# Kernel tuning notes

Hardware: AMD Instinct MI355X
Metric: run time of the kernel (lower is better)

The kernel has to match this reference:

```python
import jax, jax.numpy as jnp
import numpy as np

HEADS = 16
DIM_HEAD = 64
SCALE = float(np.sqrt(DIM_HEAD))  # NOTE: original code MULTIPLIES by sqrt(dim_head)


def setup_inputs() -> dict:
    key = jax.random.key(0)
    k1, k2, k3, k4 = jax.random.split(key, 4)
    dim = 1024
    b, n = 2, 2048
    s = 1.0 / np.sqrt(dim)
    return {
        "x": jax.random.normal(k1, (b, n, dim), dtype=jnp.float32),
        "w_q": jax.random.normal(k2, (dim, HEADS * DIM_HEAD), dtype=jnp.float32) * s,
        "w_vk": jax.random.normal(k3, (dim, HEADS * DIM_HEAD * 2), dtype=jnp.float32) * s,
        "w_out": jax.random.normal(k4, (HEADS * DIM_HEAD, dim), dtype=jnp.float32) * s,
    }


def reference(x, w_q, w_vk, w_out):
    b, n, _ = x.shape
    h, d = HEADS, DIM_HEAD
    context = x  # context=None, kv_include_self=False
    q = (x @ w_q).reshape(b, n, h, d).transpose(0, 2, 1, 3)          # b h n d
    kv = context @ w_vk                                              # b n 2hd
    k, v = jnp.split(kv, 2, axis=-1)                                 # chunk order: k first, v second
    k = k.reshape(b, n, h, d).transpose(0, 2, 1, 3)
    v = v.reshape(b, n, h, d).transpose(0, 2, 1, 3)
    dots = jnp.einsum('bhid,bhjd->bhij', q, k) * SCALE               # faithful: multiply by sqrt(d)
    attn = jax.nn.softmax(dots, axis=-1)                             # dropout p=0 -> identity
    out = jnp.einsum('bhij,bhjd->bhid', attn, v)
    out = out.transpose(0, 2, 1, 3).reshape(b, n, h * d)
    return out @ w_out
```

## Files before the change

### kernel.cpp

```cpp
#include <hip/hip_runtime.h>

typedef _Float16 half4 __attribute__((ext_vector_type(4)));
typedef _Float16 half8 __attribute__((ext_vector_type(8)));
typedef _Float16 h2pk __attribute__((ext_vector_type(2)));
typedef float f32x2 __attribute__((ext_vector_type(2)));
typedef float f32x4 __attribute__((ext_vector_type(4)));

#define MFMA_F16K32(a, b, c) __builtin_amdgcn_mfma_f32_16x16x32_f16(a, b, c, 0, 0, 0)
#define EXP2F(x) __builtin_amdgcn_exp2f(x)
#define CVT_PK(a, b) __builtin_bit_cast(h2pk, __builtin_amdgcn_cvt_pkrtz(a, b))
#define LO2(v) __builtin_shufflevector(v, v, 0, 1)
#define HI2(v) __builtin_shufflevector(v, v, 2, 3)

__device__ __forceinline__ f32x2 pk_add(f32x2 a, f32x2 b) {
  f32x2 d;
  asm("v_pk_add_f32 %0, %1, %2" : "=v"(d) : "v"(a), "v"(b));
  return d;
}
__device__ __forceinline__ f32x2 pk_mul(f32x2 a, f32x2 b) {
  f32x2 d;
  asm("v_pk_mul_f32 %0, %1, %2" : "=v"(d) : "v"(a), "v"(b));
  return d;
}

constexpr int NSEQ = 2048, DIM = 1024;
constexpr float QSCALE = 11.5415603271f;

__device__ __forceinline__ void ld_lds16(void* lds, const void* g) {
  __builtin_amdgcn_global_load_lds(
      (const __attribute__((address_space(1))) void*)g,
      (__attribute__((address_space(3))) void*)lds, 16, 0, 0);
}

__global__ __launch_bounds__(256) void prep(
    const float* __restrict__ w_q, const float* __restrict__ w_vk,
    const float* __restrict__ w_out, const float* __restrict__ x,
    _Float16* __restrict__ WT, _Float16* __restrict__ WoT,
    _Float16* __restrict__ xf) {
  const int bid = blockIdx.x;
  const int t = threadIdx.x;
  if (bid >= 1024) {
    const size_t i = ((size_t)(bid - 1024) * 256 + t) * 8;
    float4 a = *(const float4*)(x + i), b2 = *(const float4*)(x + i + 4);
    float v[8] = {a.x, a.y, a.z, a.w, b2.x, b2.y, b2.z, b2.w};
    half8 h;
#pragma unroll
    for (int j = 0; j < 8; ++j) h[j] = (_Float16)v[j];
    *(half8*)(xf + i) = h;
    return;
  }
  __shared__ float T[64][65];
  const int bx = bid & 63, k0 = (bid >> 6) * 64;
  const float* src;
  int srcN, n0, dstrow, mode;
  float scale;
  if (bx < 16) {
    src = w_q; srcN = 1024; n0 = bx * 64; dstrow = n0; scale = QSCALE; mode = 0;
  } else if (bx < 48) {
    src = w_vk; srcN = 2048; n0 = (bx - 16) * 64; dstrow = 1024 + n0;
    scale = 1.0f; mode = 0;
  } else {
    src = w_out; srcN = 1024; n0 = (bx - 48) * 64; dstrow = n0;
    scale = 1.0f; mode = 1;
  }
  {
    const int r = t >> 2, c4 = (t & 3) * 16;
    const float* s = src + (size_t)(k0 + r) * srcN + n0 + c4;
    float4 v0 = ((const float4*)s)[0], v1 = ((const float4*)s)[1],
           v2 = ((const float4*)s)[2], v3 = ((const float4*)s)[3];
    *(float4*)&T[r][c4 + 0] = v0;  *(float4*)&T[r][c4 + 4] = v1;
    *(float4*)&T[r][c4 + 8] = v2;  *(float4*)&T[r][c4 + 12] = v3;
  }
  __syncthreads();
  const int rn = t >> 2, kc = (t & 3) * 16;
  half8 hv[2];
#pragma unroll
  for (int hh = 0; hh < 2; ++hh)
#pragma unroll
    for (int j = 0; j < 8; ++j)
      hv[hh][j] = (_Float16)(T[kc + hh * 8 + j][rn] * scale);
  _Float16* d = ((mode == 0) ? WT + (size_t)(dstrow + rn) * 1024
                             : WoT + (size_t)(n0 + rn) * 1024) + k0 + kc;
  *(half8*)d = hv[0]; *(half8*)(d + 8) = hv[1];
}

__global__ __launch_bounds__(256, 4) void proj6(
    const _Float16* __restrict__ xf, const _Float16* __restrict__ WT,
    _Float16* __restrict__ qb, _Float16* __restrict__ kb,
    _Float16* __restrict__ VT) {
  __shared__ __align__(16) char smem[32768];
  const int t = threadIdx.x;
  const int lane = t & 63, wave = t >> 6, quad = lane >> 4, lq = lane & 15;
  const int wid0 = blockIdx.x + 24 * blockIdx.y;
  const int wid = (wid0 & 7) * 96 + (wid0 >> 3);
  const int bn = (wid % 24) * 128, bm = (wid / 24) * 128;
  const int kind = bn >> 10;
  const int wm = (wave >> 1) * 64, wn = (wave & 1) * 64;

  const int srow = lane >> 2;
  const int schk = (lane & 3) ^ (srow & 3);
  const _Float16* xg = xf + (size_t)(bm + wave * 32 + srow) * DIM + schk * 8;
  const _Float16* bg = WT + (size_t)(bn + wave * 32 + srow) * DIM + schk * 8;
  const int wb = wave * 2048;

  auto issue = [&](char* buf, int k0) {
    ld_lds16(buf + wb,                xg + k0);
    ld_lds16(buf + wb + 1024,         xg + k0 + 16 * DIM);
    ld_lds16(buf + 8192 + wb,         bg + k0);
    ld_lds16(buf + 8192 + wb + 1024,  bg + k0 + 16 * DIM);
  };

  const int swz = (quad ^ (lq & 3)) * 8;

  f32x4 acc[4][4];
#pragma unroll
  for (int i = 0; i < 4; ++i)
#pragma unroll
    for (int j = 0; j < 4; ++j) acc[i][j] = (f32x4){0.f, 0.f, 0.f, 0.f};

  char* bufA = smem;
  char* bufB = smem + 16384;
  issue(bufA, 0);
  if (kind == 2) {
    for (int k0 = 0; k0 < DIM; k0 += 32) {
      char* cur = ((k0 >> 5) & 1) ? bufB : bufA;
      char* nxt = ((k0 >> 5) & 1) ? bufA : bufB;
      __syncthreads();
      if (k0 + 32 < DIM) issue(nxt, k0 + 32);
      const _Float16* Xs = (const _Float16*)cur;
      const _Float16* Bs = (const _Float16*)(cur + 8192);
      half8 ah[4];
#pragma unroll
      for (int i = 0; i < 4; ++i)
        ah[i] = *(const half8*)&Xs[(wm + i * 16 + lq) * 32 + swz];
#pragma unroll
      for (int j = 0; j < 4; ++j) {
        half8 bf = *(const half8*)&Bs[(wn + j * 16 + lq) * 32 + swz];
#pragma unroll
        for (int i = 0; i < 4; ++i)
          acc[i][j] = MFMA_F16K32(ah[i], bf, acc[i][j]);
      }
    }
  } else {
    for (int k0 = 0; k0 < DIM; k0 += 32) {
      char* cur = ((k0 >> 5) & 1) ? bufB : bufA;
      char* nxt = ((k0 >> 5) & 1) ? bufA : bufB;
      __syncthreads();
      if (k0 + 32 < DIM) issue(nxt, k0 + 32);
      const _Float16* Xs = (const _Float16*)cur;
      const _Float16* Bs = (const _Float16*)(cur + 8192);
      half8 ah[4];
#pragma unroll
      for (int i = 0; i < 4; ++i)
        ah[i] = *(const half8*)&Xs[(wm + i * 16 + lq) * 32 + swz];
#pragma unroll
      for (int j = 0; j < 4; ++j) {
        half8 bf = *(const half8*)&Bs[(wn + j * 16 + lq) * 32 + swz];
#pragma unroll
        for (int i = 0; i < 4; ++i)
          acc[i][j] = MFMA_F16K32(bf, ah[i], acc[i][j]);
      }
    }
  }

  if (kind == 2) {
    _Float16* Ols = (_Float16*)smem;
    const int cb = bn - 2048;
    __syncthreads();
#pragma unroll
    for (int pass = 0; pass < 2; ++pass) {
      if ((wave >> 1) == pass) {
#pragma unroll
        for (int i = 0; i < 4; ++i)
#pragma unroll
          for (int j = 0; j < 4; ++j) {
            const int c = wn + j * 16 + lq;
            const int tl = i * 16 + quad * 4;
            half4 o;
#pragma unroll
            for (int r = 0; r < 4; ++r) o[r] = (_Float16)acc[i][j][r];
            *(half4*)&Ols[c * 68 + tl] = o;
          }
      }
      __syncthreads();
      {
        const int c = t >> 1, hf = t & 1;
        const int gcol = cb + c;
        const int tok0 = bm + pass * 64 + hf * 32;
        const int b2 = tok0 >> 11, n2 = tok0 & 2047;
        const _Float16* src = &Ols[c * 68 + hf * 32];
        half8 v0 = ((const half8*)src)[0], v1 = ((const half8*)src)[1],
              v2 = ((const half8*)src)[2], v3 = ((const half8*)src)[3];
        _Float16* dst =
            VT + ((size_t)(b2 * 16 + (gcol >> 6)) * 64 + (gcol & 63)) * 2048 + n2;
        ((half8*)dst)[0] = v0; ((half8*)dst)[1] = v1;
        ((half8*)dst)[2] = v2; ((half8*)dst)[3] = v3;
      }
      __syncthreads();
    }
  } else {
    _Float16* D = (kind == 0) ? qb : kb;
    const int cb = bn & 1023;
#pragma unroll
    for (int i = 0; i < 4; ++i) {
      const int row = bm + wm + i * 16 + lq;
#pragma unroll
      for (int j = 0; j < 4; ++j) {
        const int col = cb + wn + j * 16 + quad * 4;
        half4 o;
#pragma unroll
        for (int r = 0; r < 4; ++r) o[r] = (_Float16)acc[i][j][r];
        *(half4*)&D[(size_t)row * 1024 + col] = o;
      }
    }
  }
}

__global__ __launch_bounds__(512, 4) void attn12(
    const _Float16* __restrict__ qb, const _Float16* __restrict__ kb,
    const _Float16* __restrict__ vT, _Float16* __restrict__ ho) {
  __shared__ __align__(16) char smem[65536];
  const int t = threadIdx.x;
  const int lane = t & 63, wave = t >> 6, quad = lane >> 4, lq = lane & 15;
  const int group = wave >> 2, wq = wave & 3;
  const int wid = blockIdx.x + 16 * blockIdx.y;
  const int xcd = wid & 7, slot = wid >> 3;
  const int i0 = (slot & 15) * 128;
  const int bh = xcd + 8 * (slot >> 4);
  const int b = bh >> 4, head = bh & 15;
  const size_t rowbase = (size_t)b * NSEQ;

  half8 qf[2][2];
#pragma unroll
  for (int qt = 0; qt < 2; ++qt) {
    const _Float16* qp =
        qb + (rowbase + i0 + wq * 32 + qt * 16 + lq) * DIM + head * 64 + quad * 8;
    qf[qt][0] = *(const half8*)qp;
    qf[qt][1] = *(const half8*)(qp + 32);
  }

  f32x4 o[2][4];
#pragma unroll
  for (int qt = 0; qt < 2; ++qt)
#pragma unroll
    for (int dt = 0; dt < 4; ++dt) o[qt][dt] = (f32x4){0.f, 0.f, 0.f, 0.f};
  float mrun[2] = {-3.0e38f, -3.0e38f};
  float lrun[2] = {0.f, 0.f};

  const int srow = lane >> 3, schk = (lane & 7) ^ srow;
  const int krow = (wq >> 1) * 32 + (wq & 1) * 4 + ((srow & 4) << 1) + (srow & 3);
  const _Float16* kgp =
      kb + (rowbase + krow) * DIM + head * 64 + schk * 8;
  const int vrow = lane >> 3;
  const int vchk = (lane & 7) ^ vrow;
  const _Float16* vgp =
      vT + ((size_t)bh * 64 + wq * 16 + vrow) * 2048 + vchk * 8;

  auto issue = [&](int bsel, int j) {
    char* kd = smem + (group * 2 + bsel) * 8192 + wq * 2048;
    char* vd = kd + 32768;
    ld_lds16(kd,        kgp + (size_t)(j)      * DIM);
    ld_lds16(kd + 1024, kgp + (size_t)(j + 16) * DIM);
    ld_lds16(vd,        vgp + j);
    ld_lds16(vd + 1024, vgp + 8 * 2048 + j);
  };

  const int swzK0 = (quad ^ (lq & 7)) * 8;
  const int swzK1 = ((quad + 4) ^ (lq & 7)) * 8;

  issue(0, group * 64);

  for (int p = 0; p < 16; ++p) {
    const int cur = p & 1;
    __syncthreads();
    if (p < 15) issue(cur ^ 1, (2 * p + group) * 64 + 128);
    const _Float16* Khs = (const _Float16*)(smem + (group * 2 + cur) * 8192);
    const _Float16* Vts = (const _Float16*)(smem + 32768 + (group * 2 + cur) * 8192);

    f32x4 s[2][4];
    __builtin_amdgcn_s_setprio(1);
#pragma unroll
    for (int nt = 0; nt < 4; ++nt) {
      const int roff = (nt * 16 + lq) * 64;
      half8 k0f = *(const half8*)&Khs[roff + swzK0];
      half8 k1f = *(const half8*)&Khs[roff + swzK1];
#pragma unroll
      for (int qt = 0; qt < 2; ++qt) {
        f32x4 sv = (f32x4){0.f, 0.f, 0.f, 0.f};
        sv = MFMA_F16K32(k0f, qf[qt][0], sv);
        sv = MFMA_F16K32(k1f, qf[qt][1], sv);
        s[qt][nt] = sv;
      }
    }
    __builtin_amdgcn_s_setprio(0);

    half8 pa8[2][2];
#pragma unroll
    for (int qt = 0; qt < 2; ++qt) {
      float a0 = fmaxf(fmaxf(s[qt][0][0], s[qt][0][1]), s[qt][0][2]);
      float a1 = fmaxf(fmaxf(s[qt][0][3], s[qt][1][0]), s[qt][1][1]);
      float a2 = fmaxf(fmaxf(s[qt][1][2], s[qt][1][3]), s[qt][2][0]);
      float a3 = fmaxf(fmaxf(s[qt][2][1], s[qt][2][2]), s[qt][2][3]);
      float a4 = fmaxf(fmaxf(s[qt][3][0], s[qt][3][1]), s[qt][3][2]);
      float mx = fmaxf(fmaxf(fmaxf(a0, a1), a2),
                       fmaxf(fmaxf(a3, a4), s[qt][3][3]));
      mx = fmaxf(mx, __shfl_xor(mx, 16));
      mx = fmaxf(mx, __shfl_xor(mx, 32));
      const float mn = fmaxf(mrun[qt], mx);
      const float alpha = EXP2F(mrun[qt] - mn);
      mrun[qt] = mn;
      const float nmn = -mn;
      const f32x2 nm = {nmn, nmn};
      float rs = 0.f;
#pragma unroll
      for (int nt = 0; nt < 4; ++nt) {
        f32x2 dlo = pk_add(LO2(s[qt][nt]), nm);
        f32x2 dhi = pk_add(HI2(s[qt][nt]), nm);
        float p0 = EXP2F(dlo[0]), p1 = EXP2F(dlo[1]);
        float p2 = EXP2F(dhi[0]), p3 = EXP2F(dhi[1]);
        rs += (p0 + p1) + (p2 + p3);
        h2pk lo = CVT_PK(p0, p1);
        h2pk hi = CVT_PK(p2, p3);
        const int bb = nt >> 1, e = (nt & 1) * 4;
        pa8[qt][bb][e + 0] = lo[0]; pa8[qt][bb][e + 1] = lo[1];
        pa8[qt][bb][e + 2] = hi[0]; pa8[qt][bb][e + 3] = hi[1];
      }
      rs += __shfl_xor(rs, 16);
      rs += __shfl_xor(rs, 32);
      lrun[qt] = lrun[qt] * alpha + rs;
      const f32x2 af = {alpha, alpha};
#pragma unroll
      for (int dt = 0; dt < 4; ++dt) {
        f32x2 olo = pk_mul(LO2(o[qt][dt]), af);
        f32x2 ohi = pk_mul(HI2(o[qt][dt]), af);
        f32x4 on;
        on[0] = olo[0]; on[1] = olo[1]; on[2] = ohi[0]; on[3] = ohi[1];
        o[qt][dt] = on;
      }
    }

    __builtin_amdgcn_s_setprio(1);
#pragma unroll
    for (int dt = 0; dt < 4; ++dt) {
      const int vr2 = (dt * 16 + lq) * 64;
#pragma unroll
      for (int bb = 0; bb < 2; ++bb) {
        const int voff = vr2 + (((bb * 4 + quad) ^ (lq & 7)) * 8);
        half8 va = *(const half8*)&Vts[voff];
        o[0][dt] = MFMA_F16K32(va, pa8[0][bb], o[0][dt]);
        o[1][dt] = MFMA_F16K32(va, pa8[1][bb], o[1][dt]);
      }
    }
    __builtin_amdgcn_s_setprio(0);
  }

  float* dump = (float*)smem;
  __syncthreads();
  if (group == 1) {
    float* D = dump + wq * 2304 + lane * 36;
#pragma unroll
    for (int qt = 0; qt < 2; ++qt)
#pragma unroll
      for (int dt = 0; dt < 4; ++dt)
        *(f32x4*)(D + (qt * 4 + dt) * 4) = o[qt][dt];
    D[32] = mrun[0]; D[33] = lrun[0]; D[34] = mrun[1]; D[35] = lrun[1];
  }
  __syncthreads();
  _Float16* Ots = (_Float16*)(smem + 40960);
  if (group == 0) {
    const float* D = dump + wq * 2304 + lane * 36;
#pragma unroll
    for (int qt = 0; qt < 2; ++qt) {
      const float m2 = D[32 + qt * 2], l2 = D[33 + qt * 2];
      const float mM = fmaxf(mrun[qt], m2);
      const float f1 = EXP2F(mrun[qt] - mM);
      const float f2 = EXP2F(m2 - mM);
      const float inv = 1.0f / (lrun[qt] * f1 + l2 * f2);
#pragma unroll
      for (int dt = 0; dt < 4; ++dt) {
        f32x4 o2 = *(const f32x4*)(D + (qt * 4 + dt) * 4);
#pragma unroll
        for (int r = 0; r < 4; ++r) {
          const float val = (o[qt][dt][r] * f1 + o2[r] * f2) * inv;
          Ots[(wq * 32 + qt * 16 + lq) * 80 + dt * 16 + quad * 4 + r] =
              (_Float16)val;
        }
      }
    }
  }
  __syncthreads();
  {
    const int row = t >> 2, seg = t & 3;
    const _Float16* src = &Ots[row * 80 + seg * 16];
    half8 o0 = ((const half8*)src)[0], o1 = ((const half8*)src)[1];
    _Float16* dst = ho + (rowbase + i0 + row) * DIM + head * 64 + seg * 16;
    ((half8*)dst)[0] = o0; ((half8*)dst)[1] = o1;
  }
}

__global__ __launch_bounds__(256, 4) void gemm_out(
    const _Float16* __restrict__ A, const _Float16* __restrict__ BT,
    float* __restrict__ C) {
  __shared__ __align__(16) char smem[24576];
  const int t = threadIdx.x;
  const int lane = t & 63, wave = t >> 6, quad = lane >> 4, lq = lane & 15;
  const int wid0 = blockIdx.x + 8 * blockIdx.y;
  const int wid = (wid0 & 7) * 64 + (wid0 >> 3);
  const int bn = (wid % 8) * 128, bm = (wid / 8) * 64;
  const int wm = (wave >> 1) * 32, wn = (wave & 1) * 64;

  const int bco = (lane & 7) ^ (lane >> 3);
  const int brow = 2 * (lane >> 3) + (bco >> 2);
  const int bcc = bco & 3;
  const _Float16* ag = A + (size_t)(bm + wave * 16 + brow) * DIM + bcc * 8;
  const _Float16* bg = BT + (size_t)(bn + wave * 32 + brow) * DIM + bcc * 8;
  const int swzB = ((((lq & 1) << 2) | quad) ^ ((lq >> 1) & 7)) * 8;

  auto issue = [&](char* buf, int k0) {
    ld_lds16(buf + wave * 1024,               ag + k0);
    ld_lds16(buf + 4096 + wave * 2048,        bg + k0);
    ld_lds16(buf + 4096 + wave * 2048 + 1024, bg + k0 + 16 * DIM);
  };

  f32x4 acc[2][4];
#pragma unroll
  for (int i = 0; i < 2; ++i)
#pragma unroll
    for (int j = 0; j < 4; ++j) acc[i][j] = (f32x4){0.f, 0.f, 0.f, 0.f};

  char* bufA = smem;
  char* bufB = smem + 12288;
  issue(bufA, 0);
  for (int k0 = 0; k0 < DIM; k0 += 32) {
    char* cur = ((k0 >> 5) & 1) ? bufB : bufA;
    char* nxt = ((k0 >> 5) & 1) ? bufA : bufB;
    __syncthreads();
    if (k0 + 32 < DIM) issue(nxt, k0 + 32);
    const _Float16* Ahs = (const _Float16*)cur;
    const _Float16* Bhs = (const _Float16*)(cur + 4096);
    half8 ah[2];
#pragma unroll
    for (int i = 0; i < 2; ++i) {
      const int row = wm + i * 16 + lq;
      ah[i] = *(const half8*)&Ahs[(row >> 1) * 64 + swzB];
    }
#pragma unroll
    for (int j = 0; j < 4; ++j) {
      const int row = wn + j * 16 + lq;
      half8 bf = *(const half8*)&Bhs[(row >> 1) * 64 + swzB];
#pragma unroll
      for (int i = 0; i < 2; ++i)
        acc[i][j] = MFMA_F16K32(bf, ah[i], acc[i][j]);
    }
  }
#pragma unroll
  for (int i = 0; i < 2; ++i) {
    const int row = bm + wm + i * 16 + lq;
#pragma unroll
    for (int j = 0; j < 4; ++j) {
      const int col = bn + wn + j * 16 + quad * 4;
      *(f32x4*)&C[(size_t)row * 1024 + col] = acc[i][j];
    }
  }
}

extern "C" void kernel_launch(void* const* d_in, const int* in_sizes, int n_in,
                              void* d_out, int out_size, void* d_ws,
                              size_t ws_size, hipStream_t stream) {
  const float* x     = (const float*)d_in[0];
  const float* w_q   = (const float*)d_in[1];
  const float* w_vk  = (const float*)d_in[2];
  const float* w_out = (const float*)d_in[3];
  float* out = (float*)d_out;

  char* w = (char*)d_ws;
  _Float16* wT  = (_Float16*)(w);
  _Float16* woT = (_Float16*)(w + (6ull << 20));
  _Float16* qbb = (_Float16*)(w + (8ull << 20));
  _Float16* kbb = (_Float16*)(w + (16ull << 20));
  _Float16* vTb = (_Float16*)(w + (24ull << 20));
  _Float16* hob = (_Float16*)(w + (32ull << 20));
  _Float16* xfb = (_Float16*)(w + (40ull << 20));

  dim3 blk(256);
  prep<<<dim3(3072), blk, 0, stream>>>(w_q, w_vk, w_out, x, wT, woT, xfb);
  proj6<<<dim3(24, 32), blk, 0, stream>>>(xfb, wT, qbb, kbb, vTb);
  attn12<<<dim3(16, 32), dim3(512), 0, stream>>>(qbb, kbb, vTb, hob);
  gemm_out<<<dim3(8, 64), blk, 0, stream>>>(hob, woT, out);
}
```

Baseline: 178.1 us.

## Load K and V fragments directly from global memory instead of LDS staging

The attention kernel no longer stages K and V tiles through double-buffered shared memory with async global-to-LDS loads and per-iteration barriers. Each wave now reads its MFMA operand fragments straight from global memory (through the caches), and the shared buffer is shrunk to what the final cross-group reduction needs. This removes the __syncthreads per tile and the LDS traffic. In exchange, K/V are re-fetched redundantly by every wave, loads lose their prefetch overlap, and the V reads hit strided 16-byte accesses.

```diff
diff --git a/kernel.cpp b/kernel.cpp
--- a/kernel.cpp
+++ b/kernel.cpp
@@ -216,10 +216,10 @@
   }
 }
 
-__global__ __launch_bounds__(512, 4) void attn12(
+__global__ __launch_bounds__(512, 4) void attn13(
     const _Float16* __restrict__ qb, const _Float16* __restrict__ kb,
     const _Float16* __restrict__ vT, _Float16* __restrict__ ho) {
-  __shared__ __align__(16) char smem[65536];
+  __shared__ __align__(16) char smem[61440];
   const int t = threadIdx.x;
   const int lane = t & 63, wave = t >> 6, quad = lane >> 4, lq = lane & 15;
   const int group = wave >> 2, wq = wave & 3;
@@ -247,43 +247,21 @@
   float mrun[2] = {-3.0e38f, -3.0e38f};
   float lrun[2] = {0.f, 0.f};
 
-  const int srow = lane >> 3, schk = (lane & 7) ^ srow;
-  const int krow = (wq >> 1) * 32 + (wq & 1) * 4 + ((srow & 4) << 1) + (srow & 3);
-  const _Float16* kgp =
-      kb + (rowbase + krow) * DIM + head * 64 + schk * 8;
-  const int vrow = lane >> 3;
-  const int vchk = (lane & 7) ^ vrow;
-  const _Float16* vgp =
-      vT + ((size_t)bh * 64 + wq * 16 + vrow) * 2048 + vchk * 8;
-
-  auto issue = [&](int bsel, int j) {
-    char* kd = smem + (group * 2 + bsel) * 8192 + wq * 2048;
-    char* vd = kd + 32768;
-    ld_lds16(kd,        kgp + (size_t)(j)      * DIM);
-    ld_lds16(kd + 1024, kgp + (size_t)(j + 16) * DIM);
-    ld_lds16(vd,        vgp + j);
-    ld_lds16(vd + 1024, vgp + 8 * 2048 + j);
-  };
-
-  const int swzK0 = (quad ^ (lq & 7)) * 8;
-  const int swzK1 = ((quad + 4) ^ (lq & 7)) * 8;
-
-  issue(0, group * 64);
+  const int kbase = ((lq & 12) << 1) + (lq & 3);
+  const _Float16* kf0 = kb + (rowbase + kbase) * DIM + head * 64 + quad * 8;
+  const _Float16* vf0 = vT + ((size_t)bh * 64 + lq) * 2048 + quad * 8;
 
   for (int p = 0; p < 16; ++p) {
-    const int cur = p & 1;
-    __syncthreads();
-    if (p < 15) issue(cur ^ 1, (2 * p + group) * 64 + 128);
-    const _Float16* Khs = (const _Float16*)(smem + (group * 2 + cur) * 8192);
-    const _Float16* Vts = (const _Float16*)(smem + 32768 + (group * 2 + cur) * 8192);
+    const int j0 = (2 * p + group) * 64;
 
     f32x4 s[2][4];
     __builtin_amdgcn_s_setprio(1);
 #pragma unroll
     for (int nt = 0; nt < 4; ++nt) {
-      const int roff = (nt * 16 + lq) * 64;
-      half8 k0f = *(const half8*)&Khs[roff + swzK0];
-      half8 k1f = *(const half8*)&Khs[roff + swzK1];
+      const _Float16* kr =
+          kf0 + (size_t)(j0 + (nt >> 1) * 32 + (nt & 1) * 4) * DIM;
+      half8 k0f = *(const half8*)kr;
+      half8 k1f = *(const half8*)(kr + 32);
 #pragma unroll
       for (int qt = 0; qt < 2; ++qt) {
         f32x4 sv = (f32x4){0.f, 0.f, 0.f, 0.f};
@@ -342,11 +320,10 @@
     __builtin_amdgcn_s_setprio(1);
 #pragma unroll
     for (int dt = 0; dt < 4; ++dt) {
-      const int vr2 = (dt * 16 + lq) * 64;
+      const _Float16* vr = vf0 + (size_t)(dt * 16) * 2048 + j0;
 #pragma unroll
       for (int bb = 0; bb < 2; ++bb) {
-        const int voff = vr2 + (((bb * 4 + quad) ^ (lq & 7)) * 8);
-        half8 va = *(const half8*)&Vts[voff];
+        half8 va = *(const half8*)(vr + bb * 32);
         o[0][dt] = MFMA_F16K32(va, pa8[0][bb], o[0][dt]);
         o[1][dt] = MFMA_F16K32(va, pa8[1][bb], o[1][dt]);
       }
@@ -485,6 +462,6 @@
   dim3 blk(256);
   prep<<<dim3(3072), blk, 0, stream>>>(w_q, w_vk, w_out, x, wT, woT, xfb);
   proj6<<<dim3(24, 32), blk, 0, stream>>>(xfb, wT, qbb, kbb, vTb);
-  attn12<<<dim3(16, 32), dim3(512), 0, stream>>>(qbb, kbb, vTb, hob);
+  attn13<<<dim3(16, 32), dim3(512), 0, stream>>>(qbb, kbb, vTb, hob);
   gemm_out<<<dim3(8, 64), blk, 0, stream>>>(hob, woT, out);
 }
```

New measurement: 249.8 us. +40.3%, slower.

## Replace split-KV wave groups with 256-row query tiles and 128-key blocks

Applied to the files above, without the earlier changes.

Each attention block now covers 256 query rows, one per 32-row wave across all 8 waves, instead of 128 rows split across two wave groups that each processed half of the keys. Every wave walks the full key sequence in 128-key steps with a single shared double-buffered K/V tile. This removes the cross-group softmax merge through shared memory and halves how often K/V are loaded per query row. In exchange it launches half as many blocks, holds more score registers per wave, and lowers the occupancy hint from 4 to 2.

```diff
diff --git a/kernel.cpp b/kernel.cpp
--- a/kernel.cpp
+++ b/kernel.cpp
@@ -216,17 +216,16 @@
   }
 }
 
-__global__ __launch_bounds__(512, 4) void attn12(
+__global__ __launch_bounds__(512, 2) void attn14(
     const _Float16* __restrict__ qb, const _Float16* __restrict__ kb,
     const _Float16* __restrict__ vT, _Float16* __restrict__ ho) {
   __shared__ __align__(16) char smem[65536];
   const int t = threadIdx.x;
   const int lane = t & 63, wave = t >> 6, quad = lane >> 4, lq = lane & 15;
-  const int group = wave >> 2, wq = wave & 3;
-  const int wid = blockIdx.x + 16 * blockIdx.y;
+  const int wid = blockIdx.x + 8 * blockIdx.y;
   const int xcd = wid & 7, slot = wid >> 3;
-  const int i0 = (slot & 15) * 128;
-  const int bh = xcd + 8 * (slot >> 4);
+  const int i0 = (slot & 7) * 256;
+  const int bh = xcd + 8 * (slot >> 3);
   const int b = bh >> 4, head = bh & 15;
   const size_t rowbase = (size_t)b * NSEQ;
 
@@ -234,7 +233,7 @@
 #pragma unroll
   for (int qt = 0; qt < 2; ++qt) {
     const _Float16* qp =
-        qb + (rowbase + i0 + wq * 32 + qt * 16 + lq) * DIM + head * 64 + quad * 8;
+        qb + (rowbase + i0 + wave * 32 + qt * 16 + lq) * DIM + head * 64 + quad * 8;
     qf[qt][0] = *(const half8*)qp;
     qf[qt][1] = *(const half8*)(qp + 32);
   }
@@ -248,39 +247,43 @@
   float lrun[2] = {0.f, 0.f};
 
   const int srow = lane >> 3, schk = (lane & 7) ^ srow;
-  const int krow = (wq >> 1) * 32 + (wq & 1) * 4 + ((srow & 4) << 1) + (srow & 3);
+  const int wq = wave & 3;
+  const int kbase = (wave >> 2) * 64 + (wq >> 1) * 32 + (wq & 1) * 4 +
+                    ((srow & 4) << 1) + (srow & 3);
   const _Float16* kgp =
-      kb + (rowbase + krow) * DIM + head * 64 + schk * 8;
-  const int vrow = lane >> 3;
-  const int vchk = (lane & 7) ^ vrow;
-  const _Float16* vgp =
-      vT + ((size_t)bh * 64 + wq * 16 + vrow) * 2048 + vchk * 8;
-
-  auto issue = [&](int bsel, int j) {
-    char* kd = smem + (group * 2 + bsel) * 8192 + wq * 2048;
-    char* vd = kd + 32768;
-    ld_lds16(kd,        kgp + (size_t)(j)      * DIM);
-    ld_lds16(kd + 1024, kgp + (size_t)(j + 16) * DIM);
-    ld_lds16(vd,        vgp + j);
-    ld_lds16(vd + 1024, vgp + 8 * 2048 + j);
+      kb + (rowbase + kbase) * DIM + head * 64 + schk * 8;
+  const int vr = lane >> 4;
+  int vco[2];
+#pragma unroll
+  for (int is = 0; is < 2; ++is)
+    vco[is] = ((lane & 15) ^ ((is * 4 + vr) & 7)) * 8;
+  const _Float16* vgp = vT + ((size_t)bh * 64 + wave * 8 + vr) * 2048;
+
+  auto issue = [&](int bsel, int j0) {
+    char* kd = smem + bsel * 32768 + wave * 2048;
+    char* vd = smem + bsel * 32768 + 16384 + wave * 2048;
+    ld_lds16(kd,        kgp + (size_t)(j0)      * DIM);
+    ld_lds16(kd + 1024, kgp + (size_t)(j0 + 16) * DIM);
+    ld_lds16(vd,        vgp + j0 + vco[0]);
+    ld_lds16(vd + 1024, vgp + 4 * 2048 + j0 + vco[1]);
   };
 
   const int swzK0 = (quad ^ (lq & 7)) * 8;
   const int swzK1 = ((quad + 4) ^ (lq & 7)) * 8;
 
-  issue(0, group * 64);
+  issue(0, 0);
 
   for (int p = 0; p < 16; ++p) {
     const int cur = p & 1;
     __syncthreads();
-    if (p < 15) issue(cur ^ 1, (2 * p + group) * 64 + 128);
-    const _Float16* Khs = (const _Float16*)(smem + (group * 2 + cur) * 8192);
-    const _Float16* Vts = (const _Float16*)(smem + 32768 + (group * 2 + cur) * 8192);
-
-    f32x4 s[2][4];
+    if (p < 15) issue(cur ^ 1, (p + 1) * 128);
+    const _Float16* Khs = (const _Float16*)(smem + cur * 32768);
+    const _Float16* Vts = (const _Float16*)(smem + cur * 32768 + 16384);
+
+    f32x4 s[2][8];
     __builtin_amdgcn_s_setprio(1);
 #pragma unroll
-    for (int nt = 0; nt < 4; ++nt) {
+    for (int nt = 0; nt < 8; ++nt) {
       const int roff = (nt * 16 + lq) * 64;
       half8 k0f = *(const half8*)&Khs[roff + swzK0];
       half8 k1f = *(const half8*)&Khs[roff + swzK1];
@@ -294,16 +297,16 @@
     }
     __builtin_amdgcn_s_setprio(0);
 
-    half8 pa8[2][2];
+    half8 pa8[2][4];
 #pragma unroll
     for (int qt = 0; qt < 2; ++qt) {
-      float a0 = fmaxf(fmaxf(s[qt][0][0], s[qt][0][1]), s[qt][0][2]);
-      float a1 = fmaxf(fmaxf(s[qt][0][3], s[qt][1][0]), s[qt][1][1]);
-      float a2 = fmaxf(fmaxf(s[qt][1][2], s[qt][1][3]), s[qt][2][0]);
-      float a3 = fmaxf(fmaxf(s[qt][2][1], s[qt][2][2]), s[qt][2][3]);
-      float a4 = fmaxf(fmaxf(s[qt][3][0], s[qt][3][1]), s[qt][3][2]);
-      float mx = fmaxf(fmaxf(fmaxf(a0, a1), a2),
-                       fmaxf(fmaxf(a3, a4), s[qt][3][3]));
+      float m_[8];
+#pragma unroll
+      for (int nt = 0; nt < 8; ++nt)
+        m_[nt] = fmaxf(fmaxf(s[qt][nt][0], s[qt][nt][1]),
+                       fmaxf(s[qt][nt][2], s[qt][nt][3]));
+      float mx = fmaxf(fmaxf(fmaxf(m_[0], m_[1]), fmaxf(m_[2], m_[3])),
+                       fmaxf(fmaxf(m_[4], m_[5]), fmaxf(m_[6], m_[7])));
       mx = fmaxf(mx, __shfl_xor(mx, 16));
       mx = fmaxf(mx, __shfl_xor(mx, 32));
       const float mn = fmaxf(mrun[qt], mx);
@@ -313,7 +316,7 @@
       const f32x2 nm = {nmn, nmn};
       float rs = 0.f;
 #pragma unroll
-      for (int nt = 0; nt < 4; ++nt) {
+      for (int nt = 0; nt < 8; ++nt) {
         f32x2 dlo = pk_add(LO2(s[qt][nt]), nm);
         f32x2 dhi = pk_add(HI2(s[qt][nt]), nm);
         float p0 = EXP2F(dlo[0]), p1 = EXP2F(dlo[1]);
@@ -342,9 +345,9 @@
     __builtin_amdgcn_s_setprio(1);
 #pragma unroll
     for (int dt = 0; dt < 4; ++dt) {
-      const int vr2 = (dt * 16 + lq) * 64;
-#pragma unroll
-      for (int bb = 0; bb < 2; ++bb) {
+      const int vr2 = (dt * 16 + lq) * 128;
+#pragma unroll
+      for (int bb = 0; bb < 4; ++bb) {
         const int voff = vr2 + (((bb * 4 + quad) ^ (lq & 7)) * 8);
         half8 va = *(const half8*)&Vts[voff];
         o[0][dt] = MFMA_F16K32(va, pa8[0][bb], o[0][dt]);
@@ -354,47 +357,27 @@
     __builtin_amdgcn_s_setprio(0);
   }
 
-  float* dump = (float*)smem;
+  _Float16* Ots = (_Float16*)smem;
   __syncthreads();
-  if (group == 1) {
-    float* D = dump + wq * 2304 + lane * 36;
-#pragma unroll
-    for (int qt = 0; qt < 2; ++qt)
-#pragma unroll
-      for (int dt = 0; dt < 4; ++dt)
-        *(f32x4*)(D + (qt * 4 + dt) * 4) = o[qt][dt];
-    D[32] = mrun[0]; D[33] = lrun[0]; D[34] = mrun[1]; D[35] = lrun[1];
-  }
-  __syncthreads();
-  _Float16* Ots = (_Float16*)(smem + 40960);
-  if (group == 0) {
-    const float* D = dump + wq * 2304 + lane * 36;
-#pragma unroll
-    for (int qt = 0; qt < 2; ++qt) {
-      const float m2 = D[32 + qt * 2], l2 = D[33 + qt * 2];
-      const float mM = fmaxf(mrun[qt], m2);
-      const float f1 = EXP2F(mrun[qt] - mM);
-      const float f2 = EXP2F(m2 - mM);
-      const float inv = 1.0f / (lrun[qt] * f1 + l2 * f2);
-#pragma unroll
-      for (int dt = 0; dt < 4; ++dt) {
-        f32x4 o2 = *(const f32x4*)(D + (qt * 4 + dt) * 4);
-#pragma unroll
-        for (int r = 0; r < 4; ++r) {
-          const float val = (o[qt][dt][r] * f1 + o2[r] * f2) * inv;
-          Ots[(wq * 32 + qt * 16 + lq) * 80 + dt * 16 + quad * 4 + r] =
-              (_Float16)val;
-        }
-      }
-    }
+#pragma unroll
+  for (int qt = 0; qt < 2; ++qt) {
+    const float inv = 1.0f / lrun[qt];
+#pragma unroll
+    for (int dt = 0; dt < 4; ++dt)
+#pragma unroll
+      for (int r = 0; r < 4; ++r)
+        Ots[(wave * 32 + qt * 16 + lq) * 80 + dt * 16 + quad * 4 + r] =
+            (_Float16)(o[qt][dt][r] * inv);
   }
   __syncthreads();
   {
-    const int row = t >> 2, seg = t & 3;
-    const _Float16* src = &Ots[row * 80 + seg * 16];
-    half8 o0 = ((const half8*)src)[0], o1 = ((const half8*)src)[1];
-    _Float16* dst = ho + (rowbase + i0 + row) * DIM + head * 64 + seg * 16;
+    const int row = t >> 1, seg = t & 1;
+    const _Float16* src = &Ots[row * 80 + seg * 32];
+    half8 o0 = ((const half8*)src)[0], o1 = ((const half8*)src)[1],
+          o2 = ((const half8*)src)[2], o3 = ((const half8*)src)[3];
+    _Float16* dst = ho + (rowbase + i0 + row) * DIM + head * 64 + seg * 32;
     ((half8*)dst)[0] = o0; ((half8*)dst)[1] = o1;
+    ((half8*)dst)[2] = o2; ((half8*)dst)[3] = o3;
   }
 }
 
@@ -485,6 +468,6 @@
   dim3 blk(256);
   prep<<<dim3(3072), blk, 0, stream>>>(w_q, w_vk, w_out, x, wT, woT, xfb);
   proj6<<<dim3(24, 32), blk, 0, stream>>>(xfb, wT, qbb, kbb, vTb);
-  attn12<<<dim3(16, 32), dim3(512), 0, stream>>>(qbb, kbb, vTb, hob);
+  attn14<<<dim3(8, 32), dim3(512), 0, stream>>>(qbb, kbb, vTb, hob);
   gemm_out<<<dim3(8, 64), blk, 0, stream>>>(hob, woT, out);
 }
```

After: 179.1 us. No clear change (+0.6%).
